# Performance work log

Hardware: AMD Instinct MI355X
Metric: run time of the kernel (lower is better)

Reference implementation:

```python
import jax, jax.numpy as jnp
import numpy as np

B, D = 8192, 1024
GATE_BIAS = 0.0
LN_EPS = 1e-5


def _layernorm(x, w, b):
    mu = jnp.mean(x, axis=-1, keepdims=True)
    var = jnp.mean(jnp.square(x - mu), axis=-1, keepdims=True)
    return (x - mu) * jax.lax.rsqrt(var + LN_EPS) * w + b


def setup_inputs() -> dict:
    key = jax.random.key(0)
    ks = jax.random.split(key, 12)
    s_in = 1.0 / np.sqrt(2 * D)  # torch Linear init scale (fan_in = 2*dim)
    return {
        "x": jax.random.normal(ks[0], (B, D), jnp.float32),
        "h": jax.random.normal(ks[1], (B, D), jnp.float32),
        "ln_w": jnp.ones((2 * D,), jnp.float32),
        "ln_b": jnp.zeros((2 * D,), jnp.float32),
        "ln2_w": jnp.ones((2 * D,), jnp.float32),
        "ln2_b": jnp.zeros((2 * D,), jnp.float32),
        "Wg": jax.random.uniform(ks[2], (5 * D, 2 * D), jnp.float32, -s_in, s_in),
        "bg": jax.random.uniform(ks[3], (5 * D,), jnp.float32, -s_in, s_in),
        "Wu": jax.random.uniform(ks[4], (D, 2 * D), jnp.float32, -s_in, s_in),
        "bu": jax.random.uniform(ks[5], (D,), jnp.float32, -s_in, s_in),
    }


def reference(x, h, ln_w, ln_b, ln2_w, ln2_b, Wg, bg, Wu, bu):
    # eval mode: dropout / dropout_mask (ones) / zoneout are identity
    inp = jnp.concatenate([x, h], axis=1)          # [B, 2D]
    inp = _layernorm(inp, ln_w, ln_b)
    gates = inp @ Wg.T + bg                        # [B, 5D]
    g0, g1, g2, g3, g4 = jnp.split(gates, 5, axis=1)
    rx = jax.nn.sigmoid(g0)
    rh = jax.nn.sigmoid(g1)
    z = jax.nn.softmax(jnp.stack([g2, g3, g4 - GATE_BIAS], axis=-1), axis=-1)  # [B, D, 3]
    inp2 = jnp.concatenate([x * rx, h * rh], axis=1)
    inp2 = _layernorm(inp2, ln2_w, ln2_b)
    u = jnp.tanh(inp2 @ Wu.T + bu)                 # [B, D]
    h_new = (jnp.stack([x, h, u], axis=-1) * z).sum(-1)
    return h_new
```

## Files before the change

kernel.cpp:

```cpp
#include <hip/hip_runtime.h>

typedef __attribute__((ext_vector_type(8))) __bf16 bf16x8;
typedef __attribute__((ext_vector_type(4))) float f32x4;

#define B_ROWS 8192
#define D_DIM  1024
#define K_DIM  2048
#define NG     5120

typedef const __attribute__((address_space(1))) void cg_void;
typedef __attribute__((address_space(3))) void lds_void;

__device__ __forceinline__ float bf2f(unsigned short u) {
    union { unsigned int ui; float f; } c; c.ui = ((unsigned int)u) << 16; return c.f;
}
__device__ __forceinline__ unsigned short f2bf(float f) {
    unsigned int u = __float_as_uint(f);
    unsigned int r = u + 0x7fffu + ((u >> 16) & 1u);
    return (unsigned short)(r >> 16);
}
__device__ __forceinline__ float sigm(float v) { return 1.0f / (1.0f + __expf(-v)); }

__global__ __launch_bounds__(256) void cvt2_f32_bf16(const float* __restrict__ wg,
                                                     const float* __restrict__ wu,
                                                     unsigned short* __restrict__ og,
                                                     unsigned short* __restrict__ ou) {
    const int NG4 = 5120 * 2048 / 4;
    const int NU4 = 1024 * 2048 / 4;
    int i = blockIdx.x * 256 + threadIdx.x;
    if (i < NG4) {
        float4 v = reinterpret_cast<const float4*>(wg)[i];
        ushort4 o; o.x = f2bf(v.x); o.y = f2bf(v.y); o.z = f2bf(v.z); o.w = f2bf(v.w);
        reinterpret_cast<ushort4*>(og)[i] = o;
    } else if (i < NG4 + NU4) {
        int j = i - NG4;
        float4 v = reinterpret_cast<const float4*>(wu)[j];
        ushort4 o; o.x = f2bf(v.x); o.y = f2bf(v.y); o.z = f2bf(v.z); o.w = f2bf(v.w);
        reinterpret_cast<ushort4*>(ou)[j] = o;
    }
}

__global__ __launch_bounds__(256) void ln1_kernel(const float* __restrict__ x, const float* __restrict__ h,
                                                  const float* __restrict__ w, const float* __restrict__ b,
                                                  unsigned short* __restrict__ out) {
    const int row = blockIdx.x;
    const int t = threadIdx.x;
    const float4 xv = reinterpret_cast<const float4*>(x + (size_t)row * D_DIM)[t];
    const float4 hv = reinterpret_cast<const float4*>(h + (size_t)row * D_DIM)[t];
    float s  = xv.x + xv.y + xv.z + xv.w + hv.x + hv.y + hv.z + hv.w;
    float s2 = xv.x*xv.x + xv.y*xv.y + xv.z*xv.z + xv.w*xv.w
             + hv.x*hv.x + hv.y*hv.y + hv.z*hv.z + hv.w*hv.w;
#pragma unroll
    for (int off = 32; off > 0; off >>= 1) { s += __shfl_xor(s, off); s2 += __shfl_xor(s2, off); }
    __shared__ float red[8];
    const int wid = t >> 6, lane = t & 63;
    if (lane == 0) { red[wid] = s; red[4 + wid] = s2; }
    __syncthreads();
    s  = red[0] + red[1] + red[2] + red[3];
    s2 = red[4] + red[5] + red[6] + red[7];
    const float mu  = s * (1.0f / K_DIM);
    const float var = s2 * (1.0f / K_DIM) - mu * mu;
    const float inv = rsqrtf(var + 1e-5f);
    const float4 w0 = reinterpret_cast<const float4*>(w)[t];
    const float4 b0 = reinterpret_cast<const float4*>(b)[t];
    const float4 w1 = reinterpret_cast<const float4*>(w + D_DIM)[t];
    const float4 b1 = reinterpret_cast<const float4*>(b + D_DIM)[t];
    ushort4 o0, o1;
    o0.x = f2bf((xv.x - mu) * inv * w0.x + b0.x);
    o0.y = f2bf((xv.y - mu) * inv * w0.y + b0.y);
    o0.z = f2bf((xv.z - mu) * inv * w0.z + b0.z);
    o0.w = f2bf((xv.w - mu) * inv * w0.w + b0.w);
    o1.x = f2bf((hv.x - mu) * inv * w1.x + b1.x);
    o1.y = f2bf((hv.y - mu) * inv * w1.y + b1.y);
    o1.z = f2bf((hv.z - mu) * inv * w1.z + b1.z);
    o1.w = f2bf((hv.w - mu) * inv * w1.w + b1.w);
    reinterpret_cast<ushort4*>(out + (size_t)row * K_DIM)[t] = o0;
    reinterpret_cast<ushort4*>(out + (size_t)row * K_DIM + D_DIM)[t] = o1;
}

__global__ __launch_bounds__(256) void gate_ln2_kernel(const float* __restrict__ x, const float* __restrict__ h,
                                                       const unsigned short* __restrict__ gates,
                                                       const float* __restrict__ w, const float* __restrict__ b,
                                                       unsigned short* __restrict__ out) {
    const int row = blockIdx.x;
    const int t = threadIdx.x;
    const float4 xv = reinterpret_cast<const float4*>(x + (size_t)row * D_DIM)[t];
    const float4 hv = reinterpret_cast<const float4*>(h + (size_t)row * D_DIM)[t];
    const ushort4 g0v = reinterpret_cast<const ushort4*>(gates + (size_t)row * NG)[t];
    const ushort4 g1v = reinterpret_cast<const ushort4*>(gates + (size_t)row * NG + D_DIM)[t];
    float a0 = xv.x * sigm(bf2f(g0v.x));
    float a1 = xv.y * sigm(bf2f(g0v.y));
    float a2 = xv.z * sigm(bf2f(g0v.z));
    float a3 = xv.w * sigm(bf2f(g0v.w));
    float c0 = hv.x * sigm(bf2f(g1v.x));
    float c1 = hv.y * sigm(bf2f(g1v.y));
    float c2 = hv.z * sigm(bf2f(g1v.z));
    float c3 = hv.w * sigm(bf2f(g1v.w));
    float s  = a0 + a1 + a2 + a3 + c0 + c1 + c2 + c3;
    float s2 = a0*a0 + a1*a1 + a2*a2 + a3*a3 + c0*c0 + c1*c1 + c2*c2 + c3*c3;
#pragma unroll
    for (int off = 32; off > 0; off >>= 1) { s += __shfl_xor(s, off); s2 += __shfl_xor(s2, off); }
    __shared__ float red[8];
    const int wid = t >> 6, lane = t & 63;
    if (lane == 0) { red[wid] = s; red[4 + wid] = s2; }
    __syncthreads();
    s  = red[0] + red[1] + red[2] + red[3];
    s2 = red[4] + red[5] + red[6] + red[7];
    const float mu  = s * (1.0f / K_DIM);
    const float var = s2 * (1.0f / K_DIM) - mu * mu;
    const float inv = rsqrtf(var + 1e-5f);
    const float4 w0 = reinterpret_cast<const float4*>(w)[t];
    const float4 b0 = reinterpret_cast<const float4*>(b)[t];
    const float4 w1 = reinterpret_cast<const float4*>(w + D_DIM)[t];
    const float4 b1 = reinterpret_cast<const float4*>(b + D_DIM)[t];
    ushort4 o0, o1;
    o0.x = f2bf((a0 - mu) * inv * w0.x + b0.x);
    o0.y = f2bf((a1 - mu) * inv * w0.y + b0.y);
    o0.z = f2bf((a2 - mu) * inv * w0.z + b0.z);
    o0.w = f2bf((a3 - mu) * inv * w0.w + b0.w);
    o1.x = f2bf((c0 - mu) * inv * w1.x + b1.x);
    o1.y = f2bf((c1 - mu) * inv * w1.y + b1.y);
    o1.z = f2bf((c2 - mu) * inv * w1.z + b1.z);
    o1.w = f2bf((c3 - mu) * inv * w1.w + b1.w);
    reinterpret_cast<ushort4*>(out + (size_t)row * K_DIM)[t] = o0;
    reinterpret_cast<ushort4*>(out + (size_t)row * K_DIM + D_DIM)[t] = o1;
}

#define PH(BUF, H, KQ, LOADB, STAGE_CODE, VMCNT_CODE) do {                                            \
    bf16x8 aF[4];                                                                                     \
    _Pragma("unroll")                                                                                 \
    for (int m = 0; m < 4; ++m)                                                                       \
        aF[m] = *reinterpret_cast<const bf16x8*>(                                                     \
            &smem[((BUF) * 2 + (H)) * 8192 + ((aRdS[m] ^ ((KQ) * 64)) >> 1)]);                        \
    if (LOADB) {                                                                                      \
        _Pragma("unroll")                                                                             \
        for (int n = 0; n < 4; ++n)                                                                   \
            bF[KQ][n] = *reinterpret_cast<const bf16x8*>(                                             \
                &smem[32768 + ((BUF) * 2 + bHalf) * 8192 + ((bRdS[n] ^ ((KQ) * 64)) >> 1)]);          \
    }                                                                                                 \
    STAGE_CODE;                                                                                       \
    VMCNT_CODE;                                                                                       \
    asm volatile("" ::: "memory");                                                                    \
    __builtin_amdgcn_s_barrier();                                                                     \
    asm volatile("" ::: "memory");                                                                    \
    __builtin_amdgcn_s_setprio(1);                                                                    \
    _Pragma("unroll")                                                                                 \
    for (int m = 0; m < 4; ++m)                                                                       \
        _Pragma("unroll")                                                                             \
        for (int n = 0; n < 4; ++n)                                                                   \
            acc[(H) * 4 + m][n] =                                                                     \
                __builtin_amdgcn_mfma_f32_16x16x32_bf16(aF[m], bF[KQ][n], acc[(H) * 4 + m][n], 0, 0, 0);\
    __builtin_amdgcn_s_setprio(0);                                                                    \
    asm volatile("" ::: "memory");                                                                    \
    __builtin_amdgcn_s_barrier();                                                                     \
    asm volatile("" ::: "memory");                                                                    \
} while (0)

#define VMC4 asm volatile("s_waitcnt vmcnt(4)" ::: "memory")
#define VMC0 asm volatile("s_waitcnt vmcnt(0)" ::: "memory")
#define NOVM (void)0

__global__ __launch_bounds__(512, 2) void gemm_gates8(const unsigned short* __restrict__ A,
                                                      const unsigned short* __restrict__ W,
                                                      const float* __restrict__ bias,
                                                      unsigned short* __restrict__ C) {
    constexpr int K = K_DIM;
    constexpr int NT = K / 64;
    constexpr int NI = NT / 2;
    extern __shared__ unsigned short smem[];

    const int tid = threadIdx.x;
    const int bid = blockIdx.x;
    const int swz = (bid & 7) * 80 + (bid >> 3);
    const int tm = swz / 20;
    const int tn = swz % 20;
    const int Arow0 = tm * 256;
    const int Brow0 = tn * 256;

    const int lane = tid & 63;
    const int wid = tid >> 6;
    const int wr = wid >> 2;
    const int wc = wid & 3;
    const int fr = lane & 15;
    const int kb = lane >> 4;
    const int bHalf = wc >> 1;
    const int swzl = (fr & 7) << 4;

    int aRdS[4], bRdS[4];
#pragma unroll
    for (int m = 0; m < 4; ++m)
        aRdS[m] = (((wr * 64 + m * 16 + fr) * 128) + kb * 16) ^ swzl;
#pragma unroll
    for (int n = 0; n < 4; ++n)
        bRdS[n] = ((((wc & 1) * 64 + n * 16 + fr) * 128) + kb * 16) ^ swzl;

    size_t aSrc[2], bSrc[2];
    int ldsDst[2];
#pragma unroll
    for (int l = 0; l < 2; ++l) {
        const int off = (l * 512 + tid) * 16;
        const int r = off >> 7;
        const int offS = off ^ ((r & 7) << 4);
        const int cb = (offS & 127) >> 1;
        aSrc[l] = (size_t)(Arow0 + r) * K + cb;
        bSrc[l] = (size_t)(Brow0 + r) * K + cb;
        ldsDst[l] = (l * 512 + tid) * 8;
    }

    auto stageA = [&](int buf, int half, int kt) {
#pragma unroll
        for (int l = 0; l < 2; ++l)
            __builtin_amdgcn_global_load_lds(
                (cg_void*)(A + aSrc[l] + (size_t)half * 128 * K + kt * 64),
                (lds_void*)(&smem[(buf * 2 + half) * 8192 + ldsDst[l]]), 16, 0, 0);
    };
    auto stageB = [&](int buf, int half, int kt) {
#pragma unroll
        for (int l = 0; l < 2; ++l)
            __builtin_amdgcn_global_load_lds(
                (cg_void*)(W + bSrc[l] + (size_t)half * 128 * K + kt * 64),
                (lds_void*)(&smem[32768 + (buf * 2 + half) * 8192 + ldsDst[l]]), 16, 0, 0);
    };

    f32x4 acc[8][4] = {};

    stageA(0, 0, 0); stageA(0, 1, 0); stageB(0, 0, 0); stageB(0, 1, 0);
    stageB(1, 0, 1); stageB(1, 1, 1);
    VMC4;
    asm volatile("" ::: "memory");
    __builtin_amdgcn_s_barrier();
    asm volatile("" ::: "memory");

    for (int i = 0; i < NI; ++i) {
        const int t1 = 2 * i + 1;
        const int t2 = (2 * i + 2) & (NT - 1);
        const int t3 = (2 * i + 3) & (NT - 1);
        bf16x8 bF[2][4];
        PH(0, 0, 0, 1, { stageA(1, 0, t1); stageA(1, 1, t1); }, NOVM);
        PH(0, 0, 1, 1, ;, NOVM);
        PH(0, 1, 0, 0, { stageA(0, 0, t2); }, NOVM);
        PH(0, 1, 1, 0, { stageB(0, 0, t2); }, VMC4);
        PH(1, 0, 0, 1, { stageA(0, 1, t2); stageB(0, 1, t2); }, NOVM);
        PH(1, 0, 1, 1, ;, NOVM);
        PH(1, 1, 0, 0, { stageB(1, 0, t3); }, NOVM);
        PH(1, 1, 1, 0, { stageB(1, 1, t3); }, VMC4);
    }

    VMC0;
    asm volatile("" ::: "memory");
    __builtin_amdgcn_s_barrier();
    asm volatile("" ::: "memory");

#pragma unroll
    for (int n = 0; n < 4; ++n) {
        const int lcol = wc * 64 + n * 16 + fr;
        const float bvv = bias[Brow0 + lcol];
#pragma unroll
        for (int hh = 0; hh < 2; ++hh)
#pragma unroll
            for (int m = 0; m < 4; ++m) {
                const int lr0 = wr * 64 + hh * 128 + m * 16 + kb * 4;
#pragma unroll
                for (int j = 0; j < 4; ++j) {
                    const int lrow = lr0 + j;
                    const int byte = lrow * 512 + ((lcol * 2) ^ ((lrow & 7) << 4));
                    smem[byte >> 1] = f2bf(acc[hh * 4 + m][n][j] + bvv);
                }
            }
    }
    asm volatile("" ::: "memory");
    __builtin_amdgcn_s_barrier();
    asm volatile("" ::: "memory");

#pragma unroll
    for (int k = 0; k < 16; ++k) {
        const int cid = k * 512 + tid;
        const int row = cid >> 5;
        const int c16 = cid & 31;
        const int byte = row * 512 + ((c16 * 16) ^ ((row & 7) << 4));
        bf16x8 v = *reinterpret_cast<const bf16x8*>(&smem[byte >> 1]);
        *reinterpret_cast<bf16x8*>(&C[(size_t)(Arow0 + row) * NG + Brow0 + c16 * 8]) = v;
    }
}

__global__ __launch_bounds__(256, 3) void gemm_out3(const unsigned short* __restrict__ A,
                                                    const unsigned short* __restrict__ W,
                                                    const float* __restrict__ bias,
                                                    const unsigned short* __restrict__ gates,
                                                    const float* __restrict__ x, const float* __restrict__ h,
                                                    float* __restrict__ out) {
    constexpr int K = K_DIM;
    constexpr int NTK = K / 32;
    extern __shared__ unsigned short smem[];

    const int tid = threadIdx.x;
    const int bid = blockIdx.x;
    const int swz = (bid & 7) * 64 + (bid >> 3);
    const int tn = swz & 7;
    const int tm = swz >> 3;
    const int Arow0 = tm * 128;
    const int Brow0 = tn * 128;

    const int lane = tid & 63;
    const int wid = tid >> 6;
    const int wr = wid >> 1;
    const int wc = wid & 1;
    const int fr = lane & 15;
    const int kb = lane >> 4;

    int aRd[4], bRd[4];
#pragma unroll
    for (int m = 0; m < 4; ++m) {
        const int row = wr * 64 + m * 16 + fr;
        aRd[m] = ((row >> 1) * 128 + ((((row & 1) * 64) + kb * 16) ^ (((row >> 1) & 7) << 4))) >> 1;
    }
#pragma unroll
    for (int n = 0; n < 4; ++n) {
        const int row = wc * 64 + n * 16 + fr;
        bRd[n] = ((row >> 1) * 128 + ((((row & 1) * 64) + kb * 16) ^ (((row >> 1) & 7) << 4))) >> 1;
    }

    size_t aSrcB[2], bSrcB[2];
#pragma unroll
    for (int l = 0; l < 2; ++l) {
        const int t2 = l * 256 + tid;
        const int line = t2 >> 3;
        const int inB = (t2 & 7) * 16;
        const int inBS = inB ^ ((line & 7) << 4);
        const int row = line * 2 + (inBS >> 6);
        const int col = (inBS & 63) >> 1;
        aSrcB[l] = (size_t)(Arow0 + row) * K + col;
        bSrcB[l] = (size_t)(Brow0 + row) * K + col;
    }

    auto stage = [&](int slot, int kt) {
#pragma unroll
        for (int l = 0; l < 2; ++l)
            __builtin_amdgcn_global_load_lds((cg_void*)(A + aSrcB[l] + kt * 32),
                                             (lds_void*)(&smem[slot * 4096 + (l * 256 + tid) * 8]), 16, 0, 0);
#pragma unroll
        for (int l = 0; l < 2; ++l)
            __builtin_amdgcn_global_load_lds((cg_void*)(W + bSrcB[l] + kt * 32),
                                             (lds_void*)(&smem[12288 + slot * 4096 + (l * 256 + tid) * 8]), 16, 0, 0);
    };

    f32x4 acc[4][4] = {};

    stage(0, 0); stage(1, 1);
    VMC4;
    asm volatile("" ::: "memory");
    __builtin_amdgcn_s_barrier();
    asm volatile("" ::: "memory");

    int sC = 0;
    for (int t = 0; t < NTK; ++t) {
        const int sP = (sC == 0) ? 2 : sC - 1;
        const int kt2 = (t + 2) & (NTK - 1);

        bf16x8 aF[4], bF[4];
#pragma unroll
        for (int m = 0; m < 4; ++m)
            aF[m] = *reinterpret_cast<const bf16x8*>(&smem[sC * 4096 + aRd[m]]);
#pragma unroll
        for (int n = 0; n < 4; ++n)
            bF[n] = *reinterpret_cast<const bf16x8*>(&smem[12288 + sC * 4096 + bRd[n]]);

        stage(sP, kt2);
        VMC4;
        asm volatile("" ::: "memory");
        __builtin_amdgcn_s_barrier();
        asm volatile("" ::: "memory");

        __builtin_amdgcn_s_setprio(1);
#pragma unroll
        for (int m = 0; m < 4; ++m)
#pragma unroll
            for (int n = 0; n < 4; ++n)
                acc[m][n] = __builtin_amdgcn_mfma_f32_16x16x32_bf16(aF[m], bF[n], acc[m][n], 0, 0, 0);
        __builtin_amdgcn_s_setprio(0);
        asm volatile("" ::: "memory");
        __builtin_amdgcn_s_barrier();
        asm volatile("" ::: "memory");

        sC = (sC == 2) ? 0 : sC + 1;
    }

    const int crow0 = Arow0 + wr * 64;
    const int ccol0 = Brow0 + wc * 64;
#pragma unroll
    for (int n = 0; n < 4; ++n) {
        const int c = ccol0 + n * 16 + fr;
        const float bvv = bias[c];
#pragma unroll
        for (int m = 0; m < 4; ++m) {
            const size_t r0 = (size_t)crow0 + m * 16 + kb * 4;
#pragma unroll
            for (int j = 0; j < 4; ++j) {
                const size_t r = r0 + j;
                const float u = tanhf(acc[m][n][j] + bvv);
                const size_t gb = r * NG + c;
                const float g2 = bf2f(gates[gb + 2 * D_DIM]);
                const float g3 = bf2f(gates[gb + 3 * D_DIM]);
                const float g4 = bf2f(gates[gb + 4 * D_DIM]);
                const float mx = fmaxf(fmaxf(g2, g3), g4);
                const float e2 = __expf(g2 - mx), e3 = __expf(g3 - mx), e4 = __expf(g4 - mx);
                const float zi = 1.0f / (e2 + e3 + e4);
                const size_t xi = r * D_DIM + c;
                out[xi] = (x[xi] * e2 + h[xi] * e3 + u * e4) * zi;
            }
        }
    }
}

extern "C" void kernel_launch(void* const* d_in, const int* in_sizes, int n_in,
                              void* d_out, int out_size, void* d_ws, size_t ws_size,
                              hipStream_t stream) {
    const float* x    = (const float*)d_in[0];
    const float* h    = (const float*)d_in[1];
    const float* ln_w = (const float*)d_in[2];
    const float* ln_b = (const float*)d_in[3];
    const float* ln2_w= (const float*)d_in[4];
    const float* ln2_b= (const float*)d_in[5];
    const float* Wg   = (const float*)d_in[6];
    const float* bg   = (const float*)d_in[7];
    const float* Wu   = (const float*)d_in[8];
    const float* bu   = (const float*)d_in[9];
    float* out = (float*)d_out;

    char* ws = (char*)d_ws;
    unsigned short* inp   = (unsigned short*)(ws);
    unsigned short* Wg_b  = (unsigned short*)(ws + 33554432);
    unsigned short* Wu_b  = (unsigned short*)(ws + 33554432 + 20971520);
    unsigned short* gates = (unsigned short*)(ws + 33554432 + 20971520 + 4194304);

    (void)hipFuncSetAttribute((const void*)gemm_gates8,
                              hipFuncAttributeMaxDynamicSharedMemorySize, 131072);
    (void)hipFuncSetAttribute((const void*)gemm_out3,
                              hipFuncAttributeMaxDynamicSharedMemorySize, 49152);

    const int nCvt4 = 5120 * 2048 / 4 + 1024 * 2048 / 4;
    cvt2_f32_bf16<<<(nCvt4 + 255) / 256, 256, 0, stream>>>(Wg, Wu, Wg_b, Wu_b);
    ln1_kernel<<<8192, 256, 0, stream>>>(x, h, ln_w, ln_b, inp);
    gemm_gates8<<<640, 512, 131072, stream>>>(inp, Wg_b, bg, gates);
    gate_ln2_kernel<<<8192, 256, 0, stream>>>(x, h, gates, ln2_w, ln2_b, inp);
    gemm_out3<<<512, 256, 49152, stream>>>(inp, Wu_b, bu, gates, x, h, out);
}
```

Baseline: 316.9 us.

## Split gates GEMM tail into half-height tiles and stage output GEMM stores through LDS

```diff
diff --git a/kernel.cpp b/kernel.cpp
--- a/kernel.cpp
+++ b/kernel.cpp
@@ -156,7 +156,38 @@
     asm volatile("" ::: "memory");                                                                    \
 } while (0)
 
+#define PHH(BUF, H, KQ, LOADB, STAGE_CODE, VMCNT_CODE) do {                                           \
+    bf16x8 aFh[2];                                                                                    \
+    _Pragma("unroll")                                                                                 \
+    for (int m = 0; m < 2; ++m)                                                                       \
+        aFh[m] = *reinterpret_cast<const bf16x8*>(                                                    \
+            &smem[((BUF) * 2 + (H)) * 8192 + ((aRdH[m] ^ ((KQ) * 64)) >> 1)]);                        \
+    if (LOADB) {                                                                                      \
+        _Pragma("unroll")                                                                             \
+        for (int n = 0; n < 4; ++n)                                                                   \
+            bF[KQ][n] = *reinterpret_cast<const bf16x8*>(                                             \
+                &smem[32768 + ((BUF) * 2 + bHalf) * 8192 + ((bRdS[n] ^ ((KQ) * 64)) >> 1)]);          \
+    }                                                                                                 \
+    STAGE_CODE;                                                                                       \
+    VMCNT_CODE;                                                                                      \
+    asm volatile("" ::: "memory");                                                                    \
+    __builtin_amdgcn_s_barrier();                                                                     \
+    asm volatile("" ::: "memory");                                                                    \
+    __builtin_amdgcn_s_setprio(1);                                                                    \
+    _Pragma("unroll")                                                                                 \
+    for (int m = 0; m < 2; ++m)                                                                       \
+        _Pragma("unroll")                                                                             \
+        for (int n = 0; n < 4; ++n)                                                                   \
+            acch[(H) * 2 + m][n] =                                                                    \
+                __builtin_amdgcn_mfma_f32_16x16x32_bf16(aFh[m], bF[KQ][n], acch[(H) * 2 + m][n], 0, 0, 0);\
+    __builtin_amdgcn_s_setprio(0);                                                                    \
+    asm volatile("" ::: "memory");                                                                    \
+    __builtin_amdgcn_s_barrier();                                                                     \
+    asm volatile("" ::: "memory");                                                                    \
+} while (0)
+
 #define VMC4 asm volatile("s_waitcnt vmcnt(4)" ::: "memory")
+#define VMC3 asm volatile("s_waitcnt vmcnt(3)" ::: "memory")
 #define VMC0 asm volatile("s_waitcnt vmcnt(0)" ::: "memory")
 #define NOVM (void)0
 
@@ -171,12 +202,6 @@
 
     const int tid = threadIdx.x;
     const int bid = blockIdx.x;
-    const int swz = (bid & 7) * 80 + (bid >> 3);
-    const int tm = swz / 20;
-    const int tn = swz % 20;
-    const int Arow0 = tm * 256;
-    const int Brow0 = tn * 256;
-
     const int lane = tid & 63;
     const int wid = tid >> 6;
     const int wr = wid >> 2;
@@ -186,100 +211,216 @@
     const int bHalf = wc >> 1;
     const int swzl = (fr & 7) << 4;
 
-    int aRdS[4], bRdS[4];
-#pragma unroll
-    for (int m = 0; m < 4; ++m)
-        aRdS[m] = (((wr * 64 + m * 16 + fr) * 128) + kb * 16) ^ swzl;
-#pragma unroll
-    for (int n = 0; n < 4; ++n)
-        bRdS[n] = ((((wc & 1) * 64 + n * 16 + fr) * 128) + kb * 16) ^ swzl;
-
-    size_t aSrc[2], bSrc[2];
-    int ldsDst[2];
-#pragma unroll
-    for (int l = 0; l < 2; ++l) {
-        const int off = (l * 512 + tid) * 16;
-        const int r = off >> 7;
-        const int offS = off ^ ((r & 7) << 4);
-        const int cb = (offS & 127) >> 1;
-        aSrc[l] = (size_t)(Arow0 + r) * K + cb;
-        bSrc[l] = (size_t)(Brow0 + r) * K + cb;
-        ldsDst[l] = (l * 512 + tid) * 8;
-    }
-
-    auto stageA = [&](int buf, int half, int kt) {
-#pragma unroll
-        for (int l = 0; l < 2; ++l)
+    if (bid < 512) {
+        const int swz = (bid & 7) * 64 + (bid >> 3);
+        const int tm = swz >> 4;
+        const int tn = swz & 15;
+        const int Arow0 = tm * 256;
+        const int Brow0 = tn * 256;
+
+        int aRdS[4], bRdS[4];
+#pragma unroll
+        for (int m = 0; m < 4; ++m)
+            aRdS[m] = (((wr * 64 + m * 16 + fr) * 128) + kb * 16) ^ swzl;
+#pragma unroll
+        for (int n = 0; n < 4; ++n)
+            bRdS[n] = ((((wc & 1) * 64 + n * 16 + fr) * 128) + kb * 16) ^ swzl;
+
+        size_t aSrc[2], bSrc[2];
+        int ldsDst[2];
+#pragma unroll
+        for (int l = 0; l < 2; ++l) {
+            const int off = (l * 512 + tid) * 16;
+            const int r = off >> 7;
+            const int offS = off ^ ((r & 7) << 4);
+            const int cb = (offS & 127) >> 1;
+            aSrc[l] = (size_t)(Arow0 + r) * K + cb;
+            bSrc[l] = (size_t)(Brow0 + r) * K + cb;
+            ldsDst[l] = (l * 512 + tid) * 8;
+        }
+
+        auto stageA = [&](int buf, int half, int kt) {
+#pragma unroll
+            for (int l = 0; l < 2; ++l)
+                __builtin_amdgcn_global_load_lds(
+                    (cg_void*)(A + aSrc[l] + (size_t)half * 128 * K + kt * 64),
+                    (lds_void*)(&smem[(buf * 2 + half) * 8192 + ldsDst[l]]), 16, 0, 0);
+        };
+        auto stageB = [&](int buf, int half, int kt) {
+#pragma unroll
+            for (int l = 0; l < 2; ++l)
+                __builtin_amdgcn_global_load_lds(
+                    (cg_void*)(W + bSrc[l] + (size_t)half * 128 * K + kt * 64),
+                    (lds_void*)(&smem[32768 + (buf * 2 + half) * 8192 + ldsDst[l]]), 16, 0, 0);
+        };
+
+        f32x4 acc[8][4] = {};
+
+        stageA(0, 0, 0); stageA(0, 1, 0); stageB(0, 0, 0); stageB(0, 1, 0);
+        stageB(1, 0, 1); stageB(1, 1, 1);
+        VMC4;
+        asm volatile("" ::: "memory");
+        __builtin_amdgcn_s_barrier();
+        asm volatile("" ::: "memory");
+
+        for (int i = 0; i < NI; ++i) {
+            const int t1 = 2 * i + 1;
+            const int t2 = (2 * i + 2) & (NT - 1);
+            const int t3 = (2 * i + 3) & (NT - 1);
+            bf16x8 bF[2][4];
+            PH(0, 0, 0, 1, { stageA(1, 0, t1); stageA(1, 1, t1); }, NOVM);
+            PH(0, 0, 1, 1, ;, NOVM);
+            PH(0, 1, 0, 0, { stageA(0, 0, t2); }, NOVM);
+            PH(0, 1, 1, 0, { stageB(0, 0, t2); }, VMC4);
+            PH(1, 0, 0, 1, { stageA(0, 1, t2); stageB(0, 1, t2); }, NOVM);
+            PH(1, 0, 1, 1, ;, NOVM);
+            PH(1, 1, 0, 0, { stageB(1, 0, t3); }, NOVM);
+            PH(1, 1, 1, 0, { stageB(1, 1, t3); }, VMC4);
+        }
+
+        VMC0;
+        asm volatile("" ::: "memory");
+        __builtin_amdgcn_s_barrier();
+        asm volatile("" ::: "memory");
+
+#pragma unroll
+        for (int n = 0; n < 4; ++n) {
+            const int lcol = wc * 64 + n * 16 + fr;
+            const float bvv = bias[Brow0 + lcol];
+#pragma unroll
+            for (int hh = 0; hh < 2; ++hh)
+#pragma unroll
+                for (int m = 0; m < 4; ++m) {
+                    const int lr0 = wr * 64 + hh * 128 + m * 16 + kb * 4;
+#pragma unroll
+                    for (int j = 0; j < 4; ++j) {
+                        const int lrow = lr0 + j;
+                        const int byte = lrow * 512 + ((lcol * 2) ^ ((lrow & 7) << 4));
+                        smem[byte >> 1] = f2bf(acc[hh * 4 + m][n][j] + bvv);
+                    }
+                }
+        }
+        asm volatile("" ::: "memory");
+        __builtin_amdgcn_s_barrier();
+        asm volatile("" ::: "memory");
+#pragma unroll
+        for (int k = 0; k < 16; ++k) {
+            const int cid = k * 512 + tid;
+            const int row = cid >> 5;
+            const int c16 = cid & 31;
+            const int byte = row * 512 + ((c16 * 16) ^ ((row & 7) << 4));
+            bf16x8 v = *reinterpret_cast<const bf16x8*>(&smem[byte >> 1]);
+            *reinterpret_cast<bf16x8*>(&C[(size_t)(Arow0 + row) * NG + Brow0 + c16 * 8]) = v;
+        }
+    } else {
+        const int idx = bid - 512;
+        const int sidx = (idx & 7) * 32 + (idx >> 3);
+        const int t2i = sidx >> 1;
+        const int mhalf = sidx & 1;
+        const int tm = t2i >> 2;
+        const int tn = 16 + (t2i & 3);
+        const int Arow0 = tm * 256 + mhalf * 128;
+        const int Brow0 = tn * 256;
+
+        int aRdH[2], bRdS[4];
+#pragma unroll
+        for (int m = 0; m < 2; ++m)
+            aRdH[m] = (((wr * 32 + m * 16 + fr) * 128) + kb * 16) ^ swzl;
+#pragma unroll
+        for (int n = 0; n < 4; ++n)
+            bRdS[n] = ((((wc & 1) * 64 + n * 16 + fr) * 128) + kb * 16) ^ swzl;
+
+        size_t aSrcH;
+        {
+            const int off = tid * 16;
+            const int r = off >> 7;
+            const int offS = off ^ ((r & 7) << 4);
+            const int cb = (offS & 127) >> 1;
+            aSrcH = (size_t)(Arow0 + r) * K + cb;
+        }
+        size_t bSrc[2];
+        int ldsDst[2];
+#pragma unroll
+        for (int l = 0; l < 2; ++l) {
+            const int off = (l * 512 + tid) * 16;
+            const int r = off >> 7;
+            const int offS = off ^ ((r & 7) << 4);
+            const int cb = (offS & 127) >> 1;
+            bSrc[l] = (size_t)(Brow0 + r) * K + cb;
+            ldsDst[l] = (l * 512 + tid) * 8;
+        }
+
+        auto stageAH = [&](int buf, int half, int kt) {
             __builtin_amdgcn_global_load_lds(
-                (cg_void*)(A + aSrc[l] + (size_t)half * 128 * K + kt * 64),
-                (lds_void*)(&smem[(buf * 2 + half) * 8192 + ldsDst[l]]), 16, 0, 0);
-    };
-    auto stageB = [&](int buf, int half, int kt) {
-#pragma unroll
-        for (int l = 0; l < 2; ++l)
-            __builtin_amdgcn_global_load_lds(
-                (cg_void*)(W + bSrc[l] + (size_t)half * 128 * K + kt * 64),
-                (lds_void*)(&smem[32768 + (buf * 2 + half) * 8192 + ldsDst[l]]), 16, 0, 0);
-    };
-
-    f32x4 acc[8][4] = {};
-
-    stageA(0, 0, 0); stageA(0, 1, 0); stageB(0, 0, 0); stageB(0, 1, 0);
-    stageB(1, 0, 1); stageB(1, 1, 1);
-    VMC4;
-    asm volatile("" ::: "memory");
-    __builtin_amdgcn_s_barrier();
-    asm volatile("" ::: "memory");
-
-    for (int i = 0; i < NI; ++i) {
-        const int t1 = 2 * i + 1;
-        const int t2 = (2 * i + 2) & (NT - 1);
-        const int t3 = (2 * i + 3) & (NT - 1);
-        bf16x8 bF[2][4];
-        PH(0, 0, 0, 1, { stageA(1, 0, t1); stageA(1, 1, t1); }, NOVM);
-        PH(0, 0, 1, 1, ;, NOVM);
-        PH(0, 1, 0, 0, { stageA(0, 0, t2); }, NOVM);
-        PH(0, 1, 1, 0, { stageB(0, 0, t2); }, VMC4);
-        PH(1, 0, 0, 1, { stageA(0, 1, t2); stageB(0, 1, t2); }, NOVM);
-        PH(1, 0, 1, 1, ;, NOVM);
-        PH(1, 1, 0, 0, { stageB(1, 0, t3); }, NOVM);
-        PH(1, 1, 1, 0, { stageB(1, 1, t3); }, VMC4);
-    }
-
-    VMC0;
-    asm volatile("" ::: "memory");
-    __builtin_amdgcn_s_barrier();
-    asm volatile("" ::: "memory");
-
-#pragma unroll
-    for (int n = 0; n < 4; ++n) {
-        const int lcol = wc * 64 + n * 16 + fr;
-        const float bvv = bias[Brow0 + lcol];
-#pragma unroll
-        for (int hh = 0; hh < 2; ++hh)
-#pragma unroll
-            for (int m = 0; m < 4; ++m) {
-                const int lr0 = wr * 64 + hh * 128 + m * 16 + kb * 4;
-#pragma unroll
-                for (int j = 0; j < 4; ++j) {
-                    const int lrow = lr0 + j;
-                    const int byte = lrow * 512 + ((lcol * 2) ^ ((lrow & 7) << 4));
-                    smem[byte >> 1] = f2bf(acc[hh * 4 + m][n][j] + bvv);
+                (cg_void*)(A + aSrcH + (size_t)half * 64 * K + kt * 64),
+                (lds_void*)(&smem[(buf * 2 + half) * 8192 + tid * 8]), 16, 0, 0);
+        };
+        auto stageB = [&](int buf, int half, int kt) {
+#pragma unroll
+            for (int l = 0; l < 2; ++l)
+                __builtin_amdgcn_global_load_lds(
+                    (cg_void*)(W + bSrc[l] + (size_t)half * 128 * K + kt * 64),
+                    (lds_void*)(&smem[32768 + (buf * 2 + half) * 8192 + ldsDst[l]]), 16, 0, 0);
+        };
+
+        f32x4 acch[4][4] = {};
+
+        stageAH(0, 0, 0); stageAH(0, 1, 0); stageB(0, 0, 0); stageB(0, 1, 0);
+        stageB(1, 0, 1); stageB(1, 1, 1);
+        VMC4;
+        asm volatile("" ::: "memory");
+        __builtin_amdgcn_s_barrier();
+        asm volatile("" ::: "memory");
+
+        for (int i = 0; i < NI; ++i) {
+            const int t1 = 2 * i + 1;
+            const int t2 = (2 * i + 2) & (NT - 1);
+            const int t3 = (2 * i + 3) & (NT - 1);
+            bf16x8 bF[2][4];
+            PHH(0, 0, 0, 1, { stageAH(1, 0, t1); stageAH(1, 1, t1); }, NOVM);
+            PHH(0, 0, 1, 1, ;, NOVM);
+            PHH(0, 1, 0, 0, { stageAH(0, 0, t2); }, NOVM);
+            PHH(0, 1, 1, 0, { stageB(0, 0, t2); }, VMC3);
+            PHH(1, 0, 0, 1, { stageAH(0, 1, t2); stageB(0, 1, t2); }, NOVM);
+            PHH(1, 0, 1, 1, ;, NOVM);
+            PHH(1, 1, 0, 0, { stageB(1, 0, t3); }, NOVM);
+            PHH(1, 1, 1, 0, { stageB(1, 1, t3); }, VMC4);
+        }
+
+        VMC0;
+        asm volatile("" ::: "memory");
+        __builtin_amdgcn_s_barrier();
+        asm volatile("" ::: "memory");
+
+#pragma unroll
+        for (int n = 0; n < 4; ++n) {
+            const int lcol = wc * 64 + n * 16 + fr;
+            const float bvv = bias[Brow0 + lcol];
+#pragma unroll
+            for (int hh = 0; hh < 2; ++hh)
+#pragma unroll
+                for (int m = 0; m < 2; ++m) {
+                    const int lr0 = hh * 64 + wr * 32 + m * 16 + kb * 4;
+#pragma unroll
+                    for (int j = 0; j < 4; ++j) {
+                        const int lrow = lr0 + j;
+                        const int byte = lrow * 512 + ((lcol * 2) ^ ((lrow & 7) << 4));
+                        smem[byte >> 1] = f2bf(acch[hh * 2 + m][n][j] + bvv);
+                    }
                 }
-            }
-    }
-    asm volatile("" ::: "memory");
-    __builtin_amdgcn_s_barrier();
-    asm volatile("" ::: "memory");
-
-#pragma unroll
-    for (int k = 0; k < 16; ++k) {
-        const int cid = k * 512 + tid;
-        const int row = cid >> 5;
-        const int c16 = cid & 31;
-        const int byte = row * 512 + ((c16 * 16) ^ ((row & 7) << 4));
-        bf16x8 v = *reinterpret_cast<const bf16x8*>(&smem[byte >> 1]);
-        *reinterpret_cast<bf16x8*>(&C[(size_t)(Arow0 + row) * NG + Brow0 + c16 * 8]) = v;
+        }
+        asm volatile("" ::: "memory");
+        __builtin_amdgcn_s_barrier();
+        asm volatile("" ::: "memory");
+#pragma unroll
+        for (int k = 0; k < 8; ++k) {
+            const int cid = k * 512 + tid;
+            const int row = cid >> 5;
+            const int c16 = cid & 31;
+            const int byte = row * 512 + ((c16 * 16) ^ ((row & 7) << 4));
+            bf16x8 v = *reinterpret_cast<const bf16x8*>(&smem[byte >> 1]);
+            *reinterpret_cast<bf16x8*>(&C[(size_t)(Arow0 + row) * NG + Brow0 + c16 * 8]) = v;
+        }
     }
 }
 
@@ -385,18 +526,24 @@
         sC = (sC == 2) ? 0 : sC + 1;
     }
 
-    const int crow0 = Arow0 + wr * 64;
-    const int ccol0 = Brow0 + wc * 64;
+    VMC0;
+    asm volatile("" ::: "memory");
+    __builtin_amdgcn_s_barrier();
+    asm volatile("" ::: "memory");
+
+    float* fsm = reinterpret_cast<float*>(smem);
 #pragma unroll
     for (int n = 0; n < 4; ++n) {
-        const int c = ccol0 + n * 16 + fr;
+        const int lcol = wc * 64 + n * 16 + fr;
+        const int c = Brow0 + lcol;
         const float bvv = bias[c];
 #pragma unroll
         for (int m = 0; m < 4; ++m) {
-            const size_t r0 = (size_t)crow0 + m * 16 + kb * 4;
+            const int lr0 = wr * 64 + m * 16 + kb * 4;
 #pragma unroll
             for (int j = 0; j < 4; ++j) {
-                const size_t r = r0 + j;
+                const int lrow = lr0 + j;
+                const size_t r = (size_t)Arow0 + lrow;
                 const float u = tanhf(acc[m][n][j] + bvv);
                 const size_t gb = r * NG + c;
                 const float g2 = bf2f(gates[gb + 2 * D_DIM]);
@@ -406,9 +553,24 @@
                 const float e2 = __expf(g2 - mx), e3 = __expf(g3 - mx), e4 = __expf(g4 - mx);
                 const float zi = 1.0f / (e2 + e3 + e4);
                 const size_t xi = r * D_DIM + c;
-                out[xi] = (x[xi] * e2 + h[xi] * e3 + u * e4) * zi;
+                const float ov = (x[xi] * e2 + h[xi] * e3 + u * e4) * zi;
+                const int dw = lrow * 128 + (lcol ^ (((lrow >> 2) & 1) << 4));
+                fsm[dw] = ov;
             }
         }
+    }
+    asm volatile("" ::: "memory");
+    __builtin_amdgcn_s_barrier();
+    asm volatile("" ::: "memory");
+
+#pragma unroll
+    for (int k = 0; k < 16; ++k) {
+        const int cid = k * 256 + tid;
+        const int row = cid >> 5;
+        const int c4 = cid & 31;
+        const int dw = row * 128 + ((c4 * 4) ^ (((row >> 2) & 1) << 4));
+        float4 v = *reinterpret_cast<const float4*>(&fsm[dw]);
+        *reinterpret_cast<float4*>(&out[(size_t)(Arow0 + row) * D_DIM + Brow0 + c4 * 4]) = v;
     }
 }
 
@@ -436,12 +598,12 @@
     (void)hipFuncSetAttribute((const void*)gemm_gates8,
                               hipFuncAttributeMaxDynamicSharedMemorySize, 131072);
     (void)hipFuncSetAttribute((const void*)gemm_out3,
-                              hipFuncAttributeMaxDynamicSharedMemorySize, 49152);
+                              hipFuncAttributeMaxDynamicSharedMemorySize, 65536);
 
     const int nCvt4 = 5120 * 2048 / 4 + 1024 * 2048 / 4;
     cvt2_f32_bf16<<<(nCvt4 + 255) / 256, 256, 0, stream>>>(Wg, Wu, Wg_b, Wu_b);
     ln1_kernel<<<8192, 256, 0, stream>>>(x, h, ln_w, ln_b, inp);
-    gemm_gates8<<<640, 512, 131072, stream>>>(inp, Wg_b, bg, gates);
+    gemm_gates8<<<768, 512, 131072, stream>>>(inp, Wg_b, bg, gates);
     gate_ln2_kernel<<<8192, 256, 0, stream>>>(x, h, gates, ln2_w, ln2_b, inp);
-    gemm_out3<<<512, 256, 49152, stream>>>(inp, Wu_b, bu, gates, x, h, out);
-}
+    gemm_out3<<<512, 256, 65536, stream>>>(inp, Wu_b, bu, gates, x, h, out);
+}
```

After: 296.8 us. -6.3%, faster.
